# Performance work log

Measured on AMD Instinct MI355X. Metric: run time of the kernel, lower is better.

Reference implementation:

```python
import jax, jax.numpy as jnp
import numpy as np

ALPHA = 2.0  # ATan surrogate alpha (spikingjelly default)
V_TH = 1.0   # v_threshold
H = 8        # num_heads

@jax.custom_vjp
def atan_spike(x):
    # heaviside(v - v_th); x = v - v_th
    return (x >= 0.0).astype(x.dtype)

def _spike_fwd(x):
    return atan_spike(x), x

def _spike_bwd(x, g):
    pi_half = jnp.asarray(np.pi / 2, x.dtype)
    grad = (ALPHA / 2.0) / (1.0 + (pi_half * ALPHA * x) ** 2)
    return (g * grad,)

atan_spike.defvjp(_spike_fwd, _spike_bwd)

def lif(x_seq, w):
    # MultiStepParametricLIFNode: recurrence over leading dim of x_seq.
    # v <- v + (x - (v - v_reset)) * sigmoid(w); v_reset = 0; hard reset, detach_reset=True.
    sg = jax.nn.sigmoid(w)
    def step(v, x):
        h = v + (x - v) * sg
        s = atan_spike(h - V_TH)
        v_new = h * (1.0 - jax.lax.stop_gradient(s))  # hard reset to 0, detached spike
        return v_new, s
    v0 = jnp.zeros_like(x_seq[0])
    _, spikes = jax.lax.scan(step, v0, x_seq)
    return spikes


def setup_inputs() -> dict:
    key = jax.random.key(0)
    ks = jax.random.split(key, 6)
    T, B, N, C = 4, 32, 196, 512
    s = 0.02
    return {
        "x": jax.random.normal(ks[0], (T, B, N, C), dtype=jnp.float32),
        "Wq": jax.random.normal(ks[1], (C, C), dtype=jnp.float32) * s,
        "Wk": jax.random.normal(ks[2], (C, C), dtype=jnp.float32) * s,
        "Wv": jax.random.normal(ks[3], (C, C), dtype=jnp.float32) * s,
        "Wp": jax.random.normal(ks[4], (C, C), dtype=jnp.float32) * s,
        "bp": jax.random.normal(ks[5], (C,), dtype=jnp.float32) * s,
        "wq": jnp.zeros((), jnp.float32),  # init_tau=2 -> w=0
        "wk": jnp.zeros((), jnp.float32),
        "wv": jnp.zeros((), jnp.float32),
        "wa": jnp.zeros((), jnp.float32),
        "wp": jnp.zeros((), jnp.float32),
    }


def reference(x, Wq, Wk, Wv, Wp, bp, wq, wk, wv, wa, wp):
    T, B, N, C = x.shape
    d = C // H
    scale = d ** (-0.5)
    xf = x.reshape(T * B, N, C)  # LIF steps over T*B (faithful to original flatten(0,1))

    def qkv(W, w_lif):
        y = lif(xf @ W.T, w_lif)                       # [T*B, N, C] binary spikes
        return y.reshape(T, B, N, H, d).transpose(0, 1, 3, 2, 4)  # [T,B,H,N,d]

    q = qkv(Wq, wq)
    k = qkv(Wk, wk)
    v = qkv(Wv, wv)

    attn = jnp.einsum('tbhnd,tbhmd->tbhnm', q, k) * scale   # softmax-free
    y = jnp.einsum('tbhnm,tbhmd->tbhnd', attn, v)           # [T,B,H,N,d]
    y = y.swapaxes(3, 4).reshape(T, B, N, C)                # faithful transpose(3,4).reshape

    y = lif(y, wa)                                          # attn_lif steps over T
    out = lif(y.reshape(T * B, N, C) @ Wp.T + bp, wp)       # proj_lif steps over T*B
    return out.reshape(T, B, N, C)
```

## Files before the change

### kernel.cpp

```cpp
#include <hip/hip_runtime.h>

#define NC 100352
typedef unsigned long long ull;

template <int NMAT, bool BIAS>
__global__ __launch_bounds__(256) void gemm_nt(
    const float* __restrict__ A,
    const float* __restrict__ W0, const float* __restrict__ W1,
    const float* __restrict__ W2, const float* __restrict__ bias,
    float* __restrict__ C0, float* __restrict__ C1, float* __restrict__ C2)
{
    __shared__ float As[16][132];
    __shared__ float Bs[16][132];

    const int chunk = (NMAT * 784) >> 3;
    const int w = ((int)blockIdx.x & 7) * chunk + ((int)blockIdx.x >> 3);
    const int rp = w / (4 * NMAT);
    const int rem = w - rp * (4 * NMAT);
    const int br = rem >> 2;
    const int cb = rem & 3;

    const float* Wb = (NMAT == 1 || br == 0) ? W0 : (br == 1 ? W1 : W2);
    float* Cb = (NMAT == 1 || br == 0) ? C0 : (br == 1 ? C1 : C2);

    const int tid = threadIdx.x;
    const int r0 = tid >> 2;
    const int kq = (tid & 3) << 2;
    const int rg = (tid >> 4) << 2;
    const int cg = (tid & 15) << 2;

    float acc[8][8] = {};
    const float* A0 = A + (size_t)(rp * 128 + r0) * 512 + kq;
    const float* A1 = A0 + (size_t)64 * 512;
    const float* B0 = Wb + (size_t)(cb * 128 + r0) * 512 + kq;
    const float* B1 = B0 + (size_t)64 * 512;

    for (int k0 = 0; k0 < 512; k0 += 16) {
        const float4 a0 = *(const float4*)(A0 + k0);
        const float4 a1 = *(const float4*)(A1 + k0);
        const float4 b0 = *(const float4*)(B0 + k0);
        const float4 b1 = *(const float4*)(B1 + k0);
        __syncthreads();
        As[kq + 0][r0] = a0.x; As[kq + 1][r0] = a0.y; As[kq + 2][r0] = a0.z; As[kq + 3][r0] = a0.w;
        As[kq + 0][r0 + 64] = a1.x; As[kq + 1][r0 + 64] = a1.y; As[kq + 2][r0 + 64] = a1.z; As[kq + 3][r0 + 64] = a1.w;
        Bs[kq + 0][r0] = b0.x; Bs[kq + 1][r0] = b0.y; Bs[kq + 2][r0] = b0.z; Bs[kq + 3][r0] = b0.w;
        Bs[kq + 0][r0 + 64] = b1.x; Bs[kq + 1][r0 + 64] = b1.y; Bs[kq + 2][r0 + 64] = b1.z; Bs[kq + 3][r0 + 64] = b1.w;
        __syncthreads();
#pragma unroll
        for (int k = 0; k < 16; ++k) {
            float av[8], bv[8];
            *(float4*)&av[0] = *(const float4*)&As[k][rg];
            *(float4*)&av[4] = *(const float4*)&As[k][rg + 64];
            *(float4*)&bv[0] = *(const float4*)&Bs[k][cg];
            *(float4*)&bv[4] = *(const float4*)&Bs[k][cg + 64];
#pragma unroll
            for (int i = 0; i < 8; ++i)
#pragma unroll
                for (int j = 0; j < 8; ++j)
                    acc[i][j] = fmaf(av[i], bv[j], acc[i][j]);
        }
    }

#pragma unroll
    for (int ih = 0; ih < 2; ++ih)
#pragma unroll
        for (int i = 0; i < 4; ++i) {
            const int row = rp * 128 + rg + i + ih * 64;
#pragma unroll
            for (int jh = 0; jh < 2; ++jh) {
                const int col = cb * 128 + cg + jh * 64;
                float4 o;
                o.x = acc[ih * 4 + i][jh * 4 + 0];
                o.y = acc[ih * 4 + i][jh * 4 + 1];
                o.z = acc[ih * 4 + i][jh * 4 + 2];
                o.w = acc[ih * 4 + i][jh * 4 + 3];
                if (BIAS) {
                    o.x += bias[col + 0]; o.y += bias[col + 1];
                    o.z += bias[col + 2]; o.w += bias[col + 3];
                }
                *(float4*)&Cb[(size_t)row * 512 + col] = o;
            }
        }
}

__global__ __launch_bounds__(256) void gemm_mask(
    const uint* __restrict__ Am,
    const float* __restrict__ W, const float* __restrict__ bias,
    float* __restrict__ C)
{
    __shared__ float Bs[16][132];

    const int w = ((int)blockIdx.x & 7) * 196 + ((int)blockIdx.x >> 3);
    const int rp = w >> 2;
    const int cb = w & 3;

    const int tid = threadIdx.x;
    const int r0 = tid >> 2;
    const int kq = (tid & 3) << 2;
    const int rg = (tid >> 4) << 2;
    const int cg = (tid & 15) << 2;

    const float* B0 = W + (size_t)(cb * 128 + r0) * 512 + kq;
    const float* B1 = B0 + (size_t)64 * 512;

    const uint* mp[4];
#pragma unroll
    for (int i = 0; i < 4; ++i) {
        const int row = rp * 64 + rg + i;
        const int tb = row / 196;
        const int n = row - tb * 196;
        mp[i] = Am + (size_t)tb * 3136 + n * 16;
    }

    float acc[4][8] = {};

    for (int k0 = 0; k0 < 512; k0 += 16) {
        const float4 b0 = *(const float4*)(B0 + k0);
        const float4 b1 = *(const float4*)(B1 + k0);
        uint wv[4];
        const int wi = k0 >> 5;
        const int sh = k0 & 16;
#pragma unroll
        for (int m = 0; m < 4; ++m) wv[m] = mp[m][wi] >> sh;
        __syncthreads();
        Bs[kq + 0][r0] = b0.x; Bs[kq + 1][r0] = b0.y;
        Bs[kq + 2][r0] = b0.z; Bs[kq + 3][r0] = b0.w;
        Bs[kq + 0][r0 + 64] = b1.x; Bs[kq + 1][r0 + 64] = b1.y;
        Bs[kq + 2][r0 + 64] = b1.z; Bs[kq + 3][r0 + 64] = b1.w;
        __syncthreads();
#pragma unroll
        for (int k = 0; k < 16; ++k) {
            float bv[8], av[4];
            *(float4*)&bv[0] = *(const float4*)&Bs[k][cg];
            *(float4*)&bv[4] = *(const float4*)&Bs[k][cg + 64];
#pragma unroll
            for (int m = 0; m < 4; ++m)
                av[m] = ((wv[m] >> k) & 1u) ? 1.0f : 0.0f;
#pragma unroll
            for (int i = 0; i < 4; ++i)
#pragma unroll
                for (int j = 0; j < 8; ++j)
                    acc[i][j] = fmaf(av[i], bv[j], acc[i][j]);
        }
    }

#pragma unroll
    for (int i = 0; i < 4; ++i) {
        const int row = rp * 64 + rg + i;
#pragma unroll
        for (int jh = 0; jh < 2; ++jh) {
            const int col = cb * 128 + cg + jh * 64;
            float4 o;
            o.x = acc[i][jh * 4 + 0] + bias[col + 0];
            o.y = acc[i][jh * 4 + 1] + bias[col + 1];
            o.z = acc[i][jh * 4 + 2] + bias[col + 2];
            o.w = acc[i][jh * 4 + 3] + bias[col + 3];
            *(float4*)&C[(size_t)row * 512 + col] = o;
        }
    }
}

__global__ __launch_bounds__(256) void lif_mask3(
    const float* __restrict__ U0, const float* __restrict__ U1,
    const float* __restrict__ U2,
    const float* __restrict__ wq, const float* __restrict__ wk,
    const float* __restrict__ wv, ull* __restrict__ M)
{
    const int br = blockIdx.x / 392;
    const int blk = blockIdx.x - br * 392;
    const int i = blk * 256 + threadIdx.x;
    const float* U = (br == 0) ? U0 : (br == 1 ? U1 : U2);
    const float wv_ = (br == 0) ? wq[0] : (br == 1 ? wk[0] : wv[0]);
    const float sg = 1.0f / (1.0f + expf(-wv_));
    const bool l0 = (threadIdx.x & 63) == 0;
    ull* Mw = M + (size_t)br * 200704 + ((i >> 6) & 7) * 196 + (i >> 9);
    float v = 0.0f;
    for (int t0 = 0; t0 < 128; t0 += 4) {
        float x[4];
#pragma unroll
        for (int j = 0; j < 4; ++j) x[j] = U[(size_t)(t0 + j) * NC + i];
#pragma unroll
        for (int j = 0; j < 4; ++j) {
            const float h = __fadd_rn(v, __fmul_rn(__fsub_rn(x[j], v), sg));
            const bool sp = (h >= 1.0f);
            const ull m = __ballot(sp);
            if (l0) Mw[(size_t)(t0 + j) * 1568] = m;
            v = sp ? 0.0f : h;
        }
    }
}

__global__ __launch_bounds__(256) void lif_out(const float* __restrict__ U,
                                               const float* __restrict__ wp,
                                               float* __restrict__ out)
{
    const int i = blockIdx.x * 256 + threadIdx.x;
    const float sg = 1.0f / (1.0f + expf(-wp[0]));
    float v = 0.0f;
    for (int t0 = 0; t0 < 128; t0 += 4) {
        float x[4];
#pragma unroll
        for (int j = 0; j < 4; ++j) x[j] = U[(size_t)(t0 + j) * NC + i];
#pragma unroll
        for (int j = 0; j < 4; ++j) {
            const float h = __fadd_rn(v, __fmul_rn(__fsub_rn(x[j], v), sg));
            const bool sp = (h >= 1.0f);
            out[(size_t)(t0 + j) * NC + i] = sp ? 1.0f : 0.0f;
            v = sp ? 0.0f : h;
        }
    }
}

__global__ __launch_bounds__(512) void attn_fused(const ull* __restrict__ Qm,
                                                  const ull* __restrict__ Km,
                                                  const ull* __restrict__ Vm,
                                                  const float* __restrict__ wa,
                                                  uint* __restrict__ Ym)
{
    const int b = blockIdx.x >> 3;
    const int h = blockIdx.x & 7;
    const int tid = threadIdx.x;
    const int w = tid >> 6;
    const int lane = tid & 63;

    __shared__ ull qrow[256], krow[256], vrow[256];
    __shared__ uint kcol32[64][4][2], vcol32[64][4][2];
    __shared__ ushort G[64][64];
    __shared__ float vstate[196][64];
    __shared__ ull sbm[208];

    const float sg = 1.0f / (1.0f + expf(-wa[0]));

    for (int t = 0; t < 4; ++t) {
        const int tb = t * 32 + b;
        const size_t mb = (size_t)tb * 1568 + (size_t)h * 196;
        if (tid < 196) {
            qrow[tid] = Qm[mb + tid];
            krow[tid] = Km[mb + tid];
            vrow[tid] = Vm[mb + tid];
        } else if (tid < 256) {
            qrow[tid] = 0; krow[tid] = 0; vrow[tid] = 0;
        }
        __syncthreads();

        {
            const int j = w >> 1, half = w & 1;
            const int base = j * 64 + half * 32;
            uint kc = 0, vc = 0;
#pragma unroll 8
            for (int m = 0; m < 32; ++m) {
                kc |= (uint)((krow[base + m] >> lane) & 1ull) << m;
                vc |= (uint)((vrow[base + m] >> lane) & 1ull) << m;
            }
            kcol32[lane][j][half] = kc; vcol32[lane][j][half] = vc;
        }
        __syncthreads();

        for (int p = tid; p < 4096; p += 512) {
            const int d1 = p >> 6, d2 = p & 63;
            int g = 0;
#pragma unroll
            for (int j = 0; j < 4; ++j)
                g += __popc(kcol32[d1][j][0] & vcol32[d2][j][0]) +
                     __popc(kcol32[d1][j][1] & vcol32[d2][j][1]);
            G[d1][d2] = (ushort)g;
        }
        __syncthreads();

        {
            const int rbeg = (w * 196) >> 3;
            const int rend = ((w + 1) * 196) >> 3;
            int r = rbeg;
            for (; r + 1 < rend; r += 2) {
                const ull q0 = qrow[r], q1 = qrow[r + 1];
                const uint a0 = (uint)q0, a1 = (uint)(q0 >> 32);
                const uint b0 = (uint)q1, b1 = (uint)(q1 >> 32);
                uint s0 = 0, s1 = 0;
#pragma unroll
                for (int d = 0; d < 32; ++d) {
                    const uint g = G[d][lane];
                    s0 += ((a0 >> d) & 1u) * g;
                    s1 += ((b0 >> d) & 1u) * g;
                }
#pragma unroll
                for (int d = 0; d < 32; ++d) {
                    const uint g = G[32 + d][lane];
                    s0 += ((a1 >> d) & 1u) * g;
                    s1 += ((b1 >> d) & 1u) * g;
                }
                const float y0 = (float)s0 * 0.125f;
                const float v0 = t ? vstate[r][lane] : 0.0f;
                const float h0 = __fadd_rn(v0, __fmul_rn(__fsub_rn(y0, v0), sg));
                const bool sp0 = h0 >= 1.0f;
                vstate[r][lane] = sp0 ? 0.0f : h0;
                const ull m0 = __ballot(sp0);
                const float y1 = (float)s1 * 0.125f;
                const float v1 = t ? vstate[r + 1][lane] : 0.0f;
                const float h1 = __fadd_rn(v1, __fmul_rn(__fsub_rn(y1, v1), sg));
                const bool sp1 = h1 >= 1.0f;
                vstate[r + 1][lane] = sp1 ? 0.0f : h1;
                const ull m1 = __ballot(sp1);
                if (lane == 0) { sbm[r] = m0; sbm[r + 1] = m1; }
            }
            if (r < rend) {
                const ull q0 = qrow[r];
                const uint a0 = (uint)q0, a1 = (uint)(q0 >> 32);
                uint s0 = 0;
#pragma unroll
                for (int d = 0; d < 32; ++d) s0 += ((a0 >> d) & 1u) * (uint)G[d][lane];
#pragma unroll
                for (int d = 0; d < 32; ++d) s0 += ((a1 >> d) & 1u) * (uint)G[32 + d][lane];
                const float y0 = (float)s0 * 0.125f;
                const float v0 = t ? vstate[r][lane] : 0.0f;
                const float h0 = __fadd_rn(v0, __fmul_rn(__fsub_rn(y0, v0), sg));
                const bool sp0 = h0 >= 1.0f;
                vstate[r][lane] = sp0 ? 0.0f : h0;
                const ull m0 = __ballot(sp0);
                if (lane == 0) sbm[r] = m0;
            }
        }
        __syncthreads();

        {
            uint* Yw = Ym + (size_t)tb * 3136 + h * 392;
            for (int wd = tid; wd < 392; wd += 512) {
                const int fb = wd * 32;
                const int e0 = fb / 196;
                const int r0 = fb - e0 * 196;
                const int run = (196 - r0 >= 32) ? 32 : (196 - r0);
                uint word = 0;
                for (int j = 0; j < run; ++j)
                    word |= (uint)((sbm[r0 + j] >> e0) & 1ull) << j;
                for (int j = run; j < 32; ++j)
                    word |= (uint)((sbm[j - run] >> (e0 + 1)) & 1ull) << j;
                Yw[wd] = word;
            }
        }
        __syncthreads();
    }
}

extern "C" void kernel_launch(void* const* d_in, const int* in_sizes, int n_in,
                              void* d_out, int out_size, void* d_ws, size_t ws_size,
                              hipStream_t stream) {
    const float* x  = (const float*)d_in[0];
    const float* Wq = (const float*)d_in[1];
    const float* Wk = (const float*)d_in[2];
    const float* Wv = (const float*)d_in[3];
    const float* Wp = (const float*)d_in[4];
    const float* bp = (const float*)d_in[5];
    const float* wq = (const float*)d_in[6];
    const float* wk = (const float*)d_in[7];
    const float* wv = (const float*)d_in[8];
    const float* wa = (const float*)d_in[9];
    const float* wp = (const float*)d_in[10];
    float* out = (float*)d_out;

    char* ws = (char*)d_ws;
    float* u0 = (float*)ws;
    float* u1 = (float*)(ws + (size_t)51380224);
    float* u2 = (float*)(ws + (size_t)2 * 51380224);
    ull* Qm   = (ull*)(ws + (size_t)3 * 51380224);
    ull* Km   = Qm + 200704;
    ull* Vm   = Km + 200704;
    uint* Ym  = (uint*)(ws + (size_t)3 * 51380224 + (size_t)3 * 1605632);
    float* up = u0;

    gemm_nt<3, false><<<2352, 256, 0, stream>>>(x, Wq, Wk, Wv, nullptr,
                                                u0, u1, u2);
    lif_mask3<<<1176, 256, 0, stream>>>(u0, u1, u2, wq, wk, wv, Qm);

    attn_fused<<<256, 512, 0, stream>>>(Qm, Km, Vm, wa, Ym);

    gemm_mask<<<1568, 256, 0, stream>>>(Ym, Wp, bp, up);

    lif_out<<<392, 256, 0, stream>>>(up, wp, out);
}
```

Measured before the change: 820.2 us.

## Share A tile across Q/K/V weights in one GEMM block; widen attention block

After: 821.7 us. No clear change (+0.2%).

```diff
diff --git a/kernel.cpp b/kernel.cpp
--- a/kernel.cpp
+++ b/kernel.cpp
@@ -3,25 +3,18 @@
 #define NC 100352
 typedef unsigned long long ull;
 
-template <int NMAT, bool BIAS>
-__global__ __launch_bounds__(256) void gemm_nt(
+__global__ __launch_bounds__(256) void gemm_qkv(
     const float* __restrict__ A,
     const float* __restrict__ W0, const float* __restrict__ W1,
-    const float* __restrict__ W2, const float* __restrict__ bias,
+    const float* __restrict__ W2,
     float* __restrict__ C0, float* __restrict__ C1, float* __restrict__ C2)
 {
     __shared__ float As[16][132];
-    __shared__ float Bs[16][132];
-
-    const int chunk = (NMAT * 784) >> 3;
-    const int w = ((int)blockIdx.x & 7) * chunk + ((int)blockIdx.x >> 3);
-    const int rp = w / (4 * NMAT);
-    const int rem = w - rp * (4 * NMAT);
-    const int br = rem >> 2;
-    const int cb = rem & 3;
-
-    const float* Wb = (NMAT == 1 || br == 0) ? W0 : (br == 1 ? W1 : W2);
-    float* Cb = (NMAT == 1 || br == 0) ? C0 : (br == 1 ? C1 : C2);
+    __shared__ float Bs[3][16][68];
+
+    const int w = ((int)blockIdx.x & 7) * 196 + ((int)blockIdx.x >> 3);
+    const int rp = w >> 3;
+    const int cb = w & 7;
 
     const int tid = threadIdx.x;
     const int r0 = tid >> 2;
@@ -29,58 +22,67 @@
     const int rg = (tid >> 4) << 2;
     const int cg = (tid & 15) << 2;
 
-    float acc[8][8] = {};
-    const float* A0 = A + (size_t)(rp * 128 + r0) * 512 + kq;
-    const float* A1 = A0 + (size_t)64 * 512;
-    const float* B0 = Wb + (size_t)(cb * 128 + r0) * 512 + kq;
-    const float* B1 = B0 + (size_t)64 * 512;
+    const float* Ap0 = A + (size_t)(rp * 128 + r0) * 512 + kq;
+    const float* Ap1 = Ap0 + (size_t)64 * 512;
+    const float* Bp0 = W0 + (size_t)(cb * 64 + r0) * 512 + kq;
+    const float* Bp1 = W1 + (size_t)(cb * 64 + r0) * 512 + kq;
+    const float* Bp2 = W2 + (size_t)(cb * 64 + r0) * 512 + kq;
+
+    float acc[3][8][4] = {};
 
     for (int k0 = 0; k0 < 512; k0 += 16) {
-        const float4 a0 = *(const float4*)(A0 + k0);
-        const float4 a1 = *(const float4*)(A1 + k0);
-        const float4 b0 = *(const float4*)(B0 + k0);
-        const float4 b1 = *(const float4*)(B1 + k0);
-        __syncthreads();
-        As[kq + 0][r0] = a0.x; As[kq + 1][r0] = a0.y; As[kq + 2][r0] = a0.z; As[kq + 3][r0] = a0.w;
-        As[kq + 0][r0 + 64] = a1.x; As[kq + 1][r0 + 64] = a1.y; As[kq + 2][r0 + 64] = a1.z; As[kq + 3][r0 + 64] = a1.w;
-        Bs[kq + 0][r0] = b0.x; Bs[kq + 1][r0] = b0.y; Bs[kq + 2][r0] = b0.z; Bs[kq + 3][r0] = b0.w;
-        Bs[kq + 0][r0 + 64] = b1.x; Bs[kq + 1][r0 + 64] = b1.y; Bs[kq + 2][r0 + 64] = b1.z; Bs[kq + 3][r0 + 64] = b1.w;
+        const float4 a0 = *(const float4*)(Ap0 + k0);
+        const float4 a1 = *(const float4*)(Ap1 + k0);
+        const float4 b0 = *(const float4*)(Bp0 + k0);
+        const float4 b1 = *(const float4*)(Bp1 + k0);
+        const float4 b2 = *(const float4*)(Bp2 + k0);
+        __syncthreads();
+        As[kq + 0][r0] = a0.x; As[kq + 1][r0] = a0.y;
+        As[kq + 2][r0] = a0.z; As[kq + 3][r0] = a0.w;
+        As[kq + 0][r0 + 64] = a1.x; As[kq + 1][r0 + 64] = a1.y;
+        As[kq + 2][r0 + 64] = a1.z; As[kq + 3][r0 + 64] = a1.w;
+        Bs[0][kq + 0][r0] = b0.x; Bs[0][kq + 1][r0] = b0.y;
+        Bs[0][kq + 2][r0] = b0.z; Bs[0][kq + 3][r0] = b0.w;
+        Bs[1][kq + 0][r0] = b1.x; Bs[1][kq + 1][r0] = b1.y;
+        Bs[1][kq + 2][r0] = b1.z; Bs[1][kq + 3][r0] = b1.w;
+        Bs[2][kq + 0][r0] = b2.x; Bs[2][kq + 1][r0] = b2.y;
+        Bs[2][kq + 2][r0] = b2.z; Bs[2][kq + 3][r0] = b2.w;
         __syncthreads();
 #pragma unroll
         for (int k = 0; k < 16; ++k) {
-            float av[8], bv[8];
+            float av[8], bv0[4], bv1[4], bv2[4];
             *(float4*)&av[0] = *(const float4*)&As[k][rg];
             *(float4*)&av[4] = *(const float4*)&As[k][rg + 64];
-            *(float4*)&bv[0] = *(const float4*)&Bs[k][cg];
-            *(float4*)&bv[4] = *(const float4*)&Bs[k][cg + 64];
+            *(float4*)&bv0[0] = *(const float4*)&Bs[0][k][cg];
+            *(float4*)&bv1[0] = *(const float4*)&Bs[1][k][cg];
+            *(float4*)&bv2[0] = *(const float4*)&Bs[2][k][cg];
 #pragma unroll
             for (int i = 0; i < 8; ++i)
 #pragma unroll
-                for (int j = 0; j < 8; ++j)
-                    acc[i][j] = fmaf(av[i], bv[j], acc[i][j]);
-        }
-    }
-
-#pragma unroll
-    for (int ih = 0; ih < 2; ++ih)
-#pragma unroll
-        for (int i = 0; i < 4; ++i) {
-            const int row = rp * 128 + rg + i + ih * 64;
-#pragma unroll
-            for (int jh = 0; jh < 2; ++jh) {
-                const int col = cb * 128 + cg + jh * 64;
+                for (int j = 0; j < 4; ++j) {
+                    acc[0][i][j] = fmaf(av[i], bv0[j], acc[0][i][j]);
+                    acc[1][i][j] = fmaf(av[i], bv1[j], acc[1][i][j]);
+                    acc[2][i][j] = fmaf(av[i], bv2[j], acc[2][i][j]);
+                }
+        }
+    }
+
+#pragma unroll
+    for (int m = 0; m < 3; ++m) {
+        float* Cb = (m == 0) ? C0 : (m == 1) ? C1 : C2;
+#pragma unroll
+        for (int ih = 0; ih < 2; ++ih)
+#pragma unroll
+            for (int i = 0; i < 4; ++i) {
+                const int row = rp * 128 + rg + i + ih * 64;
                 float4 o;
-                o.x = acc[ih * 4 + i][jh * 4 + 0];
-                o.y = acc[ih * 4 + i][jh * 4 + 1];
-                o.z = acc[ih * 4 + i][jh * 4 + 2];
-                o.w = acc[ih * 4 + i][jh * 4 + 3];
-                if (BIAS) {
-                    o.x += bias[col + 0]; o.y += bias[col + 1];
-                    o.z += bias[col + 2]; o.w += bias[col + 3];
-                }
-                *(float4*)&Cb[(size_t)row * 512 + col] = o;
-            }
-        }
+                o.x = acc[m][ih * 4 + i][0];
+                o.y = acc[m][ih * 4 + i][1];
+                o.z = acc[m][ih * 4 + i][2];
+                o.w = acc[m][ih * 4 + i][3];
+                *(float4*)&Cb[(size_t)row * 512 + cb * 64 + cg] = o;
+            }
+    }
 }
 
 __global__ __launch_bounds__(256) void gemm_mask(
@@ -211,11 +213,11 @@
     }
 }
 
-__global__ __launch_bounds__(512) void attn_fused(const ull* __restrict__ Qm,
-                                                  const ull* __restrict__ Km,
-                                                  const ull* __restrict__ Vm,
-                                                  const float* __restrict__ wa,
-                                                  uint* __restrict__ Ym)
+__global__ __launch_bounds__(1024) void attn_fused(const ull* __restrict__ Qm,
+                                                   const ull* __restrict__ Km,
+                                                   const ull* __restrict__ Vm,
+                                                   const float* __restrict__ wa,
+                                                   uint* __restrict__ Ym)
 {
     const int b = blockIdx.x >> 3;
     const int h = blockIdx.x & 7;
@@ -243,7 +245,7 @@
         }
         __syncthreads();
 
-        {
+        if (w < 8) {
             const int j = w >> 1, half = w & 1;
             const int base = j * 64 + half * 32;
             uint kc = 0, vc = 0;
@@ -256,7 +258,7 @@
         }
         __syncthreads();
 
-        for (int p = tid; p < 4096; p += 512) {
+        for (int p = tid; p < 4096; p += 1024) {
             const int d1 = p >> 6, d2 = p & 63;
             int g = 0;
 #pragma unroll
@@ -268,8 +270,8 @@
         __syncthreads();
 
         {
-            const int rbeg = (w * 196) >> 3;
-            const int rend = ((w + 1) * 196) >> 3;
+            const int rbeg = (w * 196) >> 4;
+            const int rend = ((w + 1) * 196) >> 4;
             int r = rbeg;
             for (; r + 1 < rend; r += 2) {
                 const ull q0 = qrow[r], q1 = qrow[r + 1];
@@ -323,7 +325,7 @@
 
         {
             uint* Yw = Ym + (size_t)tb * 3136 + h * 392;
-            for (int wd = tid; wd < 392; wd += 512) {
+            for (int wd = tid; wd < 392; wd += 1024) {
                 const int fb = wd * 32;
                 const int e0 = fb / 196;
                 const int r0 = fb - e0 * 196;
@@ -366,11 +368,11 @@
     uint* Ym  = (uint*)(ws + (size_t)3 * 51380224 + (size_t)3 * 1605632);
     float* up = u0;
 
-    gemm_nt<3, false><<<2352, 256, 0, stream>>>(x, Wq, Wk, Wv, nullptr,
-                                                u0, u1, u2);
+    gemm_qkv<<<1568, 256, 0, stream>>>(x, Wq, Wk, Wv, u0, u1, u2);
+
     lif_mask3<<<1176, 256, 0, stream>>>(u0, u1, u2, wq, wk, wv, Qm);
 
-    attn_fused<<<256, 512, 0, stream>>>(Qm, Km, Vm, wa, Ym);
+    attn_fused<<<256, 1024, 0, stream>>>(Qm, Km, Vm, wa, Ym);
 
     gemm_mask<<<1568, 256, 0, stream>>>(Ym, Wp, bp, up);
 
```

## Enlarge QKV GEMM tile to 256x128 with double-buffered LDS; widen attention block

Applied to the files above, without the earlier changes.

New measurement: 1.225 ms. 49.4% more time.

```diff
diff --git a/kernel.cpp b/kernel.cpp
--- a/kernel.cpp
+++ b/kernel.cpp
@@ -4,19 +4,21 @@
 typedef unsigned long long ull;
 
 template <int NMAT, bool BIAS>
-__global__ __launch_bounds__(256) void gemm_nt(
+__global__ __launch_bounds__(256)
+__attribute__((amdgpu_waves_per_eu(2, 2)))
+void gemm_wpe(
     const float* __restrict__ A,
     const float* __restrict__ W0, const float* __restrict__ W1,
     const float* __restrict__ W2, const float* __restrict__ bias,
     float* __restrict__ C0, float* __restrict__ C1, float* __restrict__ C2)
 {
-    __shared__ float As[16][132];
-    __shared__ float Bs[16][132];
-
-    const int chunk = (NMAT * 784) >> 3;
+    __shared__ float As[2][16][260];
+    __shared__ float Bs[2][16][132];
+
+    const int chunk = (NMAT * 392) >> 3;
     const int w = ((int)blockIdx.x & 7) * chunk + ((int)blockIdx.x >> 3);
-    const int rp = w / (4 * NMAT);
-    const int rem = w - rp * (4 * NMAT);
+    const int mb = w / (4 * NMAT);
+    const int rem = w - mb * (4 * NMAT);
     const int br = rem >> 2;
     const int cb = rem & 3;
 
@@ -24,56 +26,88 @@
     float* Cb = (NMAT == 1 || br == 0) ? C0 : (br == 1 ? C1 : C2);
 
     const int tid = threadIdx.x;
-    const int r0 = tid >> 2;
-    const int kq = (tid & 3) << 2;
-    const int rg = (tid >> 4) << 2;
-    const int cg = (tid & 15) << 2;
-
-    float acc[8][8] = {};
-    const float* A0 = A + (size_t)(rp * 128 + r0) * 512 + kq;
-    const float* A1 = A0 + (size_t)64 * 512;
-    const float* B0 = Wb + (size_t)(cb * 128 + r0) * 512 + kq;
-    const float* B1 = B0 + (size_t)64 * 512;
-
-    for (int k0 = 0; k0 < 512; k0 += 16) {
-        const float4 a0 = *(const float4*)(A0 + k0);
-        const float4 a1 = *(const float4*)(A1 + k0);
-        const float4 b0 = *(const float4*)(B0 + k0);
-        const float4 b1 = *(const float4*)(B1 + k0);
-        __syncthreads();
-        As[kq + 0][r0] = a0.x; As[kq + 1][r0] = a0.y; As[kq + 2][r0] = a0.z; As[kq + 3][r0] = a0.w;
-        As[kq + 0][r0 + 64] = a1.x; As[kq + 1][r0 + 64] = a1.y; As[kq + 2][r0 + 64] = a1.z; As[kq + 3][r0 + 64] = a1.w;
-        Bs[kq + 0][r0] = b0.x; Bs[kq + 1][r0] = b0.y; Bs[kq + 2][r0] = b0.z; Bs[kq + 3][r0] = b0.w;
-        Bs[kq + 0][r0 + 64] = b1.x; Bs[kq + 1][r0 + 64] = b1.y; Bs[kq + 2][r0 + 64] = b1.z; Bs[kq + 3][r0 + 64] = b1.w;
-        __syncthreads();
+    const int q   = (tid & 3) << 2;
+    const int sr  = tid >> 2;
+    const int rg4 = (tid >> 4) << 2;
+    const int cg4 = (tid & 15) << 2;
+
+    const float* Ap = A  + (size_t)(mb * 256 + sr) * 512 + q;
+    const float* Bp = Wb + (size_t)(cb * 128 + sr) * 512 + q;
+
+    float acc[16][8] = {};
+    float4 a4[4], b4[2];
+
+    auto LOAD = [&](int k0) {
+#pragma unroll
+        for (int s = 0; s < 4; ++s)
+            a4[s] = *(const float4*)(Ap + (size_t)s * 64 * 512 + k0);
+#pragma unroll
+        for (int s = 0; s < 2; ++s)
+            b4[s] = *(const float4*)(Bp + (size_t)s * 64 * 512 + k0);
+    };
+    auto STORE = [&](int buf) {
+#pragma unroll
+        for (int s = 0; s < 4; ++s) {
+            As[buf][q + 0][sr + s * 64] = a4[s].x;
+            As[buf][q + 1][sr + s * 64] = a4[s].y;
+            As[buf][q + 2][sr + s * 64] = a4[s].z;
+            As[buf][q + 3][sr + s * 64] = a4[s].w;
+        }
+#pragma unroll
+        for (int s = 0; s < 2; ++s) {
+            Bs[buf][q + 0][sr + s * 64] = b4[s].x;
+            Bs[buf][q + 1][sr + s * 64] = b4[s].y;
+            Bs[buf][q + 2][sr + s * 64] = b4[s].z;
+            Bs[buf][q + 3][sr + s * 64] = b4[s].w;
+        }
+    };
+    auto COMP = [&](int buf) {
 #pragma unroll
         for (int k = 0; k < 16; ++k) {
-            float av[8], bv[8];
-            *(float4*)&av[0] = *(const float4*)&As[k][rg];
-            *(float4*)&av[4] = *(const float4*)&As[k][rg + 64];
-            *(float4*)&bv[0] = *(const float4*)&Bs[k][cg];
-            *(float4*)&bv[4] = *(const float4*)&Bs[k][cg + 64];
-#pragma unroll
-            for (int i = 0; i < 8; ++i)
+            float av[16], bv[8];
+#pragma unroll
+            for (int s = 0; s < 4; ++s)
+                *(float4*)&av[s * 4] = *(const float4*)&As[buf][k][rg4 + s * 64];
+#pragma unroll
+            for (int s = 0; s < 2; ++s)
+                *(float4*)&bv[s * 4] = *(const float4*)&Bs[buf][k][cg4 + s * 64];
+#pragma unroll
+            for (int i = 0; i < 16; ++i)
 #pragma unroll
                 for (int j = 0; j < 8; ++j)
                     acc[i][j] = fmaf(av[i], bv[j], acc[i][j]);
         }
-    }
-
-#pragma unroll
-    for (int ih = 0; ih < 2; ++ih)
+    };
+
+    LOAD(0);
+    STORE(0);
+    __syncthreads();
+    int cur = 0;
+    for (int k0 = 0; k0 < 512; k0 += 16) {
+        if (k0 + 16 < 512) {
+            LOAD(k0 + 16);
+            COMP(cur);
+            STORE(cur ^ 1);
+        } else {
+            COMP(cur);
+        }
+        __syncthreads();
+        cur ^= 1;
+    }
+
+#pragma unroll
+    for (int s = 0; s < 4; ++s)
 #pragma unroll
         for (int i = 0; i < 4; ++i) {
-            const int row = rp * 128 + rg + i + ih * 64;
-#pragma unroll
-            for (int jh = 0; jh < 2; ++jh) {
-                const int col = cb * 128 + cg + jh * 64;
+            const int row = mb * 256 + rg4 + i + s * 64;
+#pragma unroll
+            for (int half = 0; half < 2; ++half) {
+                const int col = cb * 128 + cg4 + half * 64;
                 float4 o;
-                o.x = acc[ih * 4 + i][jh * 4 + 0];
-                o.y = acc[ih * 4 + i][jh * 4 + 1];
-                o.z = acc[ih * 4 + i][jh * 4 + 2];
-                o.w = acc[ih * 4 + i][jh * 4 + 3];
+                o.x = acc[s * 4 + i][half * 4 + 0];
+                o.y = acc[s * 4 + i][half * 4 + 1];
+                o.z = acc[s * 4 + i][half * 4 + 2];
+                o.w = acc[s * 4 + i][half * 4 + 3];
                 if (BIAS) {
                     o.x += bias[col + 0]; o.y += bias[col + 1];
                     o.z += bias[col + 2]; o.w += bias[col + 3];
@@ -211,11 +245,11 @@
     }
 }
 
-__global__ __launch_bounds__(512) void attn_fused(const ull* __restrict__ Qm,
-                                                  const ull* __restrict__ Km,
-                                                  const ull* __restrict__ Vm,
-                                                  const float* __restrict__ wa,
-                                                  uint* __restrict__ Ym)
+__global__ __launch_bounds__(1024) void attn_fused(const ull* __restrict__ Qm,
+                                                   const ull* __restrict__ Km,
+                                                   const ull* __restrict__ Vm,
+                                                   const float* __restrict__ wa,
+                                                   uint* __restrict__ Ym)
 {
     const int b = blockIdx.x >> 3;
     const int h = blockIdx.x & 7;
@@ -243,7 +277,7 @@
         }
         __syncthreads();
 
-        {
+        if (w < 8) {
             const int j = w >> 1, half = w & 1;
             const int base = j * 64 + half * 32;
             uint kc = 0, vc = 0;
@@ -256,7 +290,7 @@
         }
         __syncthreads();
 
-        for (int p = tid; p < 4096; p += 512) {
+        for (int p = tid; p < 4096; p += 1024) {
             const int d1 = p >> 6, d2 = p & 63;
             int g = 0;
 #pragma unroll
@@ -268,8 +302,8 @@
         __syncthreads();
 
         {
-            const int rbeg = (w * 196) >> 3;
-            const int rend = ((w + 1) * 196) >> 3;
+            const int rbeg = (w * 196) >> 4;
+            const int rend = ((w + 1) * 196) >> 4;
             int r = rbeg;
             for (; r + 1 < rend; r += 2) {
                 const ull q0 = qrow[r], q1 = qrow[r + 1];
@@ -323,7 +357,7 @@
 
         {
             uint* Yw = Ym + (size_t)tb * 3136 + h * 392;
-            for (int wd = tid; wd < 392; wd += 512) {
+            for (int wd = tid; wd < 392; wd += 1024) {
                 const int fb = wd * 32;
                 const int e0 = fb / 196;
                 const int r0 = fb - e0 * 196;
@@ -366,11 +400,11 @@
     uint* Ym  = (uint*)(ws + (size_t)3 * 51380224 + (size_t)3 * 1605632);
     float* up = u0;
 
-    gemm_nt<3, false><<<2352, 256, 0, stream>>>(x, Wq, Wk, Wv, nullptr,
-                                                u0, u1, u2);
+    gemm_wpe<3, false><<<1176, 256, 0, stream>>>(x, Wq, Wk, Wv, nullptr,
+                                                 u0, u1, u2);
     lif_mask3<<<1176, 256, 0, stream>>>(u0, u1, u2, wq, wk, wv, Qm);
 
-    attn_fused<<<256, 512, 0, stream>>>(Qm, Km, Vm, wa, Ym);
+    attn_fused<<<256, 1024, 0, stream>>>(Qm, Km, Vm, wa, Ym);
 
     gemm_mask<<<1568, 256, 0, stream>>>(Ym, Wp, bp, up);
 
```
